# Kernel optimization log

Hardware: AMD Instinct MI355X
Metric: run time of the kernel (lower is better)

Reference implementation:

```python
import jax, jax.numpy as jnp
import numpy as np

D_MODEL = 1024
N_HEADS = 16
HEAD_DIM = D_MODEL // N_HEADS


def setup_inputs() -> dict:
    key = jax.random.key(0)
    k_x, k_qkv, k_proj = jax.random.split(key, 3)
    x = jax.random.normal(k_x, (2, 2048, D_MODEL), dtype=jnp.float32)
    # flax nnx.Linear kernels: shape (in_features, out_features), lecun_normal-ish scale
    w_qkv = jax.random.normal(k_qkv, (D_MODEL, 3 * D_MODEL), dtype=jnp.float32) / np.sqrt(D_MODEL)
    w_proj = jax.random.normal(k_proj, (D_MODEL, D_MODEL), dtype=jnp.float32) / np.sqrt(D_MODEL)
    return {"x": x, "w_qkv": w_qkv, "w_proj": w_proj}


def reference(x, w_qkv, w_proj):
    bsz, seq_len, d_model = x.shape
    qkv = x @ w_qkv  # (B, T, 3*D)
    q, k, v = jnp.split(qkv, 3, axis=-1)
    q = q.reshape(bsz, seq_len, N_HEADS, HEAD_DIM)
    k = k.reshape(bsz, seq_len, N_HEADS, HEAD_DIM)
    v = v.reshape(bsz, seq_len, N_HEADS, HEAD_DIM)
    scale = jnp.sqrt(jnp.asarray(HEAD_DIM, dtype=x.dtype))
    attn_logits = jnp.einsum('bthd,bshd->bhts', q / scale, k)  # (B, H, T, T)
    attn_weights = jax.nn.softmax(attn_logits, axis=-1)
    attn_out = jnp.einsum('bhts,bshd->bthd', attn_weights, v)
    attn_out = attn_out.reshape(bsz, seq_len, d_model)
    return attn_out @ w_proj
```

## Files before the change

kernel.cpp:

```cpp
#include <hip/hip_runtime.h>
#include <hip/hip_bf16.h>
#include <cmath>

#define D_MODEL 1024
#define NH 16
#define HD 64
#define BSZ 2
#define SEQ 2048
#define MTOT (BSZ * SEQ)

typedef _Float16 f16x8 __attribute__((ext_vector_type(8)));
typedef __fp16   fp16x2 __attribute__((ext_vector_type(2)));
typedef float    f32x4  __attribute__((ext_vector_type(4)));
typedef float    f32x16 __attribute__((ext_vector_type(16)));
typedef unsigned int uivec2 __attribute__((ext_vector_type(2)));

#define QSCALE 0.18033688011112042f

__device__ __forceinline__ ushort f2h(float x) {
    union { _Float16 h; ushort u; } cv;
    cv.h = (_Float16)x;
    return cv.u;
}
__device__ __forceinline__ uint pkh(float a, float b) {
    union { fp16x2 h; uint u; } cv;
    cv.h = __builtin_amdgcn_cvt_pkrtz(a, b);
    return cv.u;
}
__device__ __forceinline__ float fexp2(float x) {
    float r; asm("v_exp_f32 %0, %1" : "=v"(r) : "v"(x)); return r;
}
__device__ __forceinline__ float fmax3(float a, float b, float c) {
    return fmaxf(fmaxf(a, b), c);
}
__device__ __forceinline__ void gload_lds16(const ushort* g, ushort* l) {
    __builtin_amdgcn_global_load_lds(
        (const __attribute__((address_space(1))) void*)g,
        (__attribute__((address_space(3))) void*)l, 16, 0, 0);
}

__global__ __launch_bounds__(256)
void cast8(const float* __restrict__ in, ushort* __restrict__ out, int n)
{
    const int i = (blockIdx.x * 256 + threadIdx.x) * 8;
    if (i >= n) return;
    float4 a = *(const float4*)(in + i);
    float4 b = *(const float4*)(in + i + 4);
    alignas(16) ushort h8[8];
    h8[0] = f2h(a.x); h8[1] = f2h(a.y); h8[2] = f2h(a.z); h8[3] = f2h(a.w);
    h8[4] = f2h(b.x); h8[5] = f2h(b.y); h8[6] = f2h(b.z); h8[7] = f2h(b.w);
    *(uint4*)(out + i) = *(const uint4*)h8;
}

__global__ __launch_bounds__(256)
void transpose_cast2(const float* __restrict__ A, const float* __restrict__ B,
                     ushort* __restrict__ At, ushort* __restrict__ Bt)
{
    __shared__ float tile[32][33];
    const int z = blockIdx.z;
    const float* in = (z < 3) ? A : B;
    ushort* out     = (z < 3) ? At : Bt;
    const int C     = (z < 3) ? 3 * D_MODEL : D_MODEL;
    const int cb    = (z < 3) ? z * 32 + blockIdx.x : blockIdx.x;
    const int R = D_MODEL;
    const int t  = threadIdx.x;
    const int r0 = blockIdx.y * 32, c0 = cb * 32;
    const int tr = t >> 5, tc = t & 31;
#pragma unroll
    for (int s = 0; s < 4; ++s)
        tile[tr + 8 * s][tc] = in[(size_t)(r0 + tr + 8 * s) * C + c0 + tc];
    __syncthreads();
#pragma unroll
    for (int s = 0; s < 4; ++s)
        out[(size_t)(c0 + tr + 8 * s) * R + r0 + tc] = f2h(tile[tc][tr + 8 * s]);
}

template <int MODE>
__global__ __launch_bounds__(256)
void gemm_mfma(const ushort* __restrict__ A, const ushort* __restrict__ Bt,
               float* __restrict__ outp,
               ushort* __restrict__ Qw, ushort* __restrict__ Kw,
               ushort* __restrict__ Vw, int N)
{
    __shared__ ushort As[128 * 64];
    __shared__ ushort Bs[128 * 64];

    const int t  = threadIdx.x;
    const int w  = t >> 6;
    const int l  = t & 63;
    const int lr = l & 15;
    const int lg = l >> 4;
    const int wr = w >> 1, wc = w & 1;
    const int m0 = blockIdx.y * 128, n0 = blockIdx.x * 128;

    const int srow = l >> 3;
    const int scol = (l & 7) * 8;

    const ushort* Ab = A  + (size_t)m0 * 1024;
    const ushort* Bb = Bt + (size_t)n0 * 1024;

    f32x4 acc[4][4];
#pragma unroll
    for (int i = 0; i < 4; ++i)
#pragma unroll
        for (int j = 0; j < 4; ++j) acc[i][j] = (f32x4){0.f, 0.f, 0.f, 0.f};

    for (int k0 = 0; k0 < 1024; k0 += 64) {
#pragma unroll
        for (int i = 0; i < 4; ++i) {
            const int r8 = (w * 4 + i) * 8;
            gload_lds16(Ab + (size_t)(r8 + srow) * 1024 + k0 + scol, &As[r8 * 64]);
            gload_lds16(Bb + (size_t)(r8 + srow) * 1024 + k0 + scol, &Bs[r8 * 64]);
        }
        __syncthreads();

#pragma unroll
        for (int kk = 0; kk < 2; ++kk) {
            f16x8 af[4], bf[4];
#pragma unroll
            for (int m = 0; m < 4; ++m)
                af[m] = *(const f16x8*)&As[(wr * 64 + m * 16 + lr) * 64 + kk * 32 + lg * 8];
#pragma unroll
            for (int n = 0; n < 4; ++n)
                bf[n] = *(const f16x8*)&Bs[(wc * 64 + n * 16 + lr) * 64 + kk * 32 + lg * 8];
#pragma unroll
            for (int m = 0; m < 4; ++m)
#pragma unroll
                for (int n = 0; n < 4; ++n)
                    acc[m][n] = __builtin_amdgcn_mfma_f32_16x16x32_f16(
                        af[m], bf[n], acc[m][n], 0, 0, 0);
        }
        __syncthreads();
    }

    if (MODE == 1) {
#pragma unroll
        for (int mf = 0; mf < 4; ++mf) {
            const int row = m0 + wr * 64 + mf * 16 + lg * 4;
#pragma unroll
            for (int nf = 0; nf < 4; ++nf) {
                const int col = n0 + wc * 64 + nf * 16 + lr;
#pragma unroll
                for (int i = 0; i < 4; ++i)
                    outp[(size_t)(row + i) * N + col] = acc[mf][nf][i];
            }
        }
    } else {
#pragma unroll
        for (int mf = 0; mf < 4; ++mf) {
            const int row = m0 + wr * 64 + mf * 16 + lg * 4;
            const int b   = row >> 11;
            const int tt0 = row & (SEQ - 1);
#pragma unroll
            for (int nf = 0; nf < 4; ++nf) {
                const int col   = n0 + wc * 64 + nf * 16 + lr;
                const int which = col >> 10;
                const int h     = (col >> 6) & 15;
                const int d     = col & 63;
                if (which == 2) {
                    ushort* p = Vw + (((size_t)(b * NH + h) * HD + d) * SEQ) + tt0;
                    alignas(8) ushort e4[4];
#pragma unroll
                    for (int i = 0; i < 4; ++i) e4[i] = f2h(acc[mf][nf][i]);
                    *(uint2*)p = *(const uint2*)e4;
                } else {
                    ushort* dst = (which == 0) ? Qw : Kw;
                    const float sc = (which == 0) ? QSCALE : 1.0f;
#pragma unroll
                    for (int i = 0; i < 4; ++i)
                        dst[((size_t)(b * NH + h) * SEQ + tt0 + i) * HD + d] =
                            f2h(acc[mf][nf][i] * sc);
                }
            }
        }
    }
}

__global__ __launch_bounds__(512, 4)
void attn_mfma7(const ushort* __restrict__ Qw, const ushort* __restrict__ Kw,
                const ushort* __restrict__ Vtg, ushort* __restrict__ AO)
{
    __shared__ ushort KsAll[2][2][64 * 64];
    __shared__ ushort VtAll[2][2][64 * 64];

    const int t    = threadIdx.x;
    const int w    = t >> 6;
    const int l    = t & 63;
    const int q    = l & 31;
    const int hi   = l >> 5;
    const int half = w >> 2;
    const int ww   = w & 3;

    const int bh = blockIdx.y;
    const int q0 = blockIdx.x * 128 + ww * 32;
    const int kbase = half * (SEQ / 2);
    const int NT = (SEQ / 2) / 64;

    const ushort* Qp = Qw  + (size_t)bh * SEQ * HD;
    const ushort* Kp = Kw  + (size_t)bh * SEQ * HD;
    const ushort* Vp = Vtg + (size_t)bh * HD * SEQ;

    ushort (*Ks)[64 * 64] = KsAll[half];
    ushort (*Vt)[64 * 64] = VtAll[half];

    f16x8 qf[4];
#pragma unroll
    for (int kc = 0; kc < 4; ++kc)
        qf[kc] = *(const f16x8*)(Qp + (size_t)(q0 + q) * HD + kc * 16 + hi * 8);

    f32x16 oacc[2];
#pragma unroll
    for (int db = 0; db < 2; ++db)
#pragma unroll
        for (int r = 0; r < 16; ++r) oacc[db][r] = 0.f;
    float m_run = -3.0e38f, l_run = 0.f;

    auto stageK = [&](int buf, int k0) {
#pragma unroll
        for (int s = 0; s < 2; ++s) {
            const int c    = ww * 64 + l + 256 * s;
            const int row  = c >> 3;
            const int unit = (c & 7) ^ (row & 7);
            gload_lds16(Kp + (size_t)(k0 + row) * HD + unit * 8,
                        &Ks[buf][(ww * 64 + 256 * s) * 8]);
        }
    };
    auto stageV = [&](int buf, int k0) {
#pragma unroll
        for (int s = 0; s < 2; ++s) {
            const int c    = ww * 64 + l + 256 * s;
            const int row  = c >> 3;
            const int unit = (c & 7) ^ (row & 7);
            gload_lds16(Vp + (size_t)row * SEQ + k0 + unit * 8,
                        &Vt[buf][(ww * 64 + 256 * s) * 8]);
        }
    };

    stageK(0, kbase);
    stageV(0, kbase);
    __syncthreads();

    int cur = 0;
    for (int kt = 0; kt < NT; ++kt) {
        if (kt + 1 < NT) {
            stageK(cur ^ 1, kbase + (kt + 1) * 64);
            stageV(cur ^ 1, kbase + (kt + 1) * 64);
        }

        f32x16 sacc[2];
        __builtin_amdgcn_s_setprio(1);
#pragma unroll
        for (int kb = 0; kb < 2; ++kb) {
            f32x16 a;
#pragma unroll
            for (int r = 0; r < 16; ++r) a[r] = 0.f;
            const int row = kb * 32 + q;
            const int swz = (row & 7) << 4;
#pragma unroll
            for (int kc = 0; kc < 4; ++kc) {
                f16x8 kf = *(const f16x8*)(
                    (const char*)Ks[cur] + row * 128 + ((kc * 32 + hi * 16) ^ swz));
                a = __builtin_amdgcn_mfma_f32_32x32x16_f16(kf, qf[kc], a, 0, 0, 0);
            }
            sacc[kb] = a;
        }
        __builtin_amdgcn_s_setprio(0);

        float p0 = fmax3(fmaxf(sacc[0][0], sacc[1][0]),
                         fmaxf(sacc[0][1], sacc[1][1]),
                         fmaxf(sacc[0][2], sacc[1][2]));
        float p1 = fmax3(fmaxf(sacc[0][3], sacc[1][3]),
                         fmaxf(sacc[0][4], sacc[1][4]),
                         fmaxf(sacc[0][5], sacc[1][5]));
        float p2 = fmax3(fmaxf(sacc[0][6], sacc[1][6]),
                         fmaxf(sacc[0][7], sacc[1][7]),
                         fmaxf(sacc[0][8], sacc[1][8]));
        float p3 = fmax3(fmaxf(sacc[0][9], sacc[1][9]),
                         fmaxf(sacc[0][10], sacc[1][10]),
                         fmaxf(sacc[0][11], sacc[1][11]));
        float p4 = fmax3(fmaxf(sacc[0][12], sacc[1][12]),
                         fmaxf(sacc[0][13], sacc[1][13]),
                         fmaxf(sacc[0][14], sacc[1][14]));
        float p5 = fmaxf(sacc[0][15], sacc[1][15]);
        float mx = fmaxf(fmax3(p0, p1, p2), fmax3(p3, p4, p5));
        mx = fmaxf(mx, __shfl_xor(mx, 32));

        if (__any(mx > m_run + 8.0f)) {
            const float m_new = fmaxf(m_run, mx);
            const float scale = fexp2(m_run - m_new);
            m_run = m_new;
            l_run *= scale;
#pragma unroll
            for (int db = 0; db < 2; ++db)
#pragma unroll
                for (int r = 0; r < 16; ++r) oacc[db][r] *= scale;
        }

#pragma unroll
        for (int kb = 0; kb < 2; ++kb)
#pragma unroll
            for (int r = 0; r < 16; ++r)
                sacc[kb][r] = fexp2(sacc[kb][r] - m_run);

        float ts[16];
#pragma unroll
        for (int r = 0; r < 16; ++r) ts[r] = sacc[0][r] + sacc[1][r];
#pragma unroll
        for (int s = 8; s > 0; s >>= 1)
#pragma unroll
            for (int r = 0; r < 8; ++r)
                if (r < s) ts[r] += ts[r + s];
        l_run += ts[0] + __shfl_xor(ts[0], 32);

        f16x8 pfrag[4];
#pragma unroll
        for (int kb = 0; kb < 2; ++kb)
#pragma unroll
            for (int lc = 0; lc < 2; ++lc) {
                const int rb = lc * 8;
                uint a = pkh(sacc[kb][rb + 0], sacc[kb][rb + 1]);
                uint b = pkh(sacc[kb][rb + 2], sacc[kb][rb + 3]);
                uint c = pkh(sacc[kb][rb + 4], sacc[kb][rb + 5]);
                uint d = pkh(sacc[kb][rb + 6], sacc[kb][rb + 7]);
                uivec2 r0 = __builtin_amdgcn_permlane32_swap(a, c, false, false);
                uivec2 r1 = __builtin_amdgcn_permlane32_swap(b, d, false, false);
                union { uint u[4]; f16x8 v; } f;
                f.u[0] = r0.x;
                f.u[1] = r1.x;
                f.u[2] = r0.y;
                f.u[3] = r1.y;
                pfrag[kb * 2 + lc] = f.v;
            }

        __builtin_amdgcn_s_setprio(1);
#pragma unroll
        for (int db = 0; db < 2; ++db) {
            const int row = db * 32 + q;
            const int swz = (row & 7) << 4;
#pragma unroll
            for (int kc = 0; kc < 4; ++kc) {
                f16x8 vf = *(const f16x8*)(
                    (const char*)Vt[cur] + row * 128 + ((kc * 32 + hi * 16) ^ swz));
                oacc[db] = __builtin_amdgcn_mfma_f32_32x32x16_f16(
                    vf, pfrag[kc], oacc[db], 0, 0, 0);
            }
        }
        __builtin_amdgcn_s_setprio(0);

        __syncthreads();
        cur ^= 1;
    }

    float* oex = (float*)KsAll;
    float* mex = (float*)VtAll;
    float* lex = mex + 256;

    if (half == 1) {
        mex[ww * 64 + l] = m_run;
        lex[ww * 64 + l] = l_run;
#pragma unroll
        for (int db = 0; db < 2; ++db)
#pragma unroll
            for (int r = 0; r < 16; ++r)
                oex[(((ww * 2 + db) * 16) + r) * 64 + l] = oacc[db][r];
    }
    __syncthreads();
    if (half == 0) {
        const float m2 = mex[ww * 64 + l];
        const float l2 = lex[ww * 64 + l];
        const float mf = fmaxf(m_run, m2);
        float w1 = fexp2(m_run - mf), w2 = fexp2(m2 - mf);
        const float inv = 1.f / (l_run * w1 + l2 * w2);
        w1 *= inv; w2 *= inv;

        const int b = bh >> 4, h = bh & 15;
        ushort* orow = AO + ((size_t)(b * SEQ) + q0 + q) * D_MODEL + h * HD;
#pragma unroll
        for (int db = 0; db < 2; ++db)
#pragma unroll
            for (int g = 0; g < 4; ++g) {
                const int d = db * 32 + g * 8 + hi * 4;
                alignas(8) ushort e4[4];
#pragma unroll
                for (int i = 0; i < 4; ++i) {
                    const float o2 = oex[(((ww * 2 + db) * 16) + g * 4 + i) * 64 + l];
                    e4[i] = f2h(oacc[db][g * 4 + i] * w1 + o2 * w2);
                }
                *(uint2*)(orow + d) = *(const uint2*)e4;
            }
    }
}

extern "C" void kernel_launch(void* const* d_in, const int* in_sizes, int n_in,
                              void* d_out, int out_size, void* d_ws, size_t ws_size,
                              hipStream_t stream)
{
    const float* x      = (const float*)d_in[0];
    const float* w_qkv  = (const float*)d_in[1];
    const float* w_proj = (const float*)d_in[2];
    float* out = (float*)d_out;

    ushort* Xh  = (ushort*)d_ws;
    ushort* WqT = Xh  + (size_t)MTOT * D_MODEL;
    ushort* WpT = WqT + (size_t)3 * D_MODEL * D_MODEL;
    ushort* Qw  = WpT + (size_t)D_MODEL * D_MODEL;
    ushort* Kw  = Qw  + (size_t)MTOT * D_MODEL;
    ushort* Vt  = Kw  + (size_t)MTOT * D_MODEL;
    ushort* AOh = Vt  + (size_t)MTOT * D_MODEL;

    dim3 blk(256);

    cast8<<<dim3(MTOT * D_MODEL / (8 * 256)), blk, 0, stream>>>(x, Xh, MTOT * D_MODEL);
    transpose_cast2<<<dim3(32, 32, 4), blk, 0, stream>>>(w_qkv, w_proj, WqT, WpT);

    gemm_mfma<0><<<dim3(3 * D_MODEL / 128, MTOT / 128), blk, 0, stream>>>(
        Xh, WqT, nullptr, Qw, Kw, Vt, 3 * D_MODEL);

    attn_mfma7<<<dim3(SEQ / 128, BSZ * NH), dim3(512), 0, stream>>>(Qw, Kw, Vt, AOh);

    gemm_mfma<1><<<dim3(D_MODEL / 128, MTOT / 128), blk, 0, stream>>>(
        AOh, WpT, out, nullptr, nullptr, nullptr, D_MODEL);
}
```

Measured before the change: 142.5 us.

## Double-buffer GEMM LDS tiles with K=32 stages to overlap loads and MFMA

```diff
diff --git a/kernel.cpp b/kernel.cpp
--- a/kernel.cpp
+++ b/kernel.cpp
@@ -82,8 +82,8 @@
                ushort* __restrict__ Qw, ushort* __restrict__ Kw,
                ushort* __restrict__ Vw, int N)
 {
-    __shared__ ushort As[128 * 64];
-    __shared__ ushort Bs[128 * 64];
+    __shared__ ushort As[2][128 * 32];
+    __shared__ ushort Bs[2][128 * 32];
 
     const int t  = threadIdx.x;
     const int w  = t >> 6;
@@ -93,9 +93,6 @@
     const int wr = w >> 1, wc = w & 1;
     const int m0 = blockIdx.y * 128, n0 = blockIdx.x * 128;
 
-    const int srow = l >> 3;
-    const int scol = (l & 7) * 8;
-
     const ushort* Ab = A  + (size_t)m0 * 1024;
     const ushort* Bb = Bt + (size_t)n0 * 1024;
 
@@ -105,32 +102,43 @@
 #pragma unroll
         for (int j = 0; j < 4; ++j) acc[i][j] = (f32x4){0.f, 0.f, 0.f, 0.f};
 
-    for (int k0 = 0; k0 < 1024; k0 += 64) {
-#pragma unroll
-        for (int i = 0; i < 4; ++i) {
-            const int r8 = (w * 4 + i) * 8;
-            gload_lds16(Ab + (size_t)(r8 + srow) * 1024 + k0 + scol, &As[r8 * 64]);
-            gload_lds16(Bb + (size_t)(r8 + srow) * 1024 + k0 + scol, &Bs[r8 * 64]);
-        }
+    auto stage = [&](int buf, int k0) {
+#pragma unroll
+        for (int s = 0; s < 2; ++s) {
+            const int c    = s * 64 + l;
+            const int row  = w * 32 + (c >> 2);
+            const int unit = c & 3;
+            gload_lds16(Ab + (size_t)row * 1024 + k0 + unit * 8,
+                        &As[buf][(w * 128 + s * 64) * 8]);
+            gload_lds16(Bb + (size_t)row * 1024 + k0 + unit * 8,
+                        &Bs[buf][(w * 128 + s * 64) * 8]);
+        }
+    };
+
+    stage(0, 0);
+    __syncthreads();
+
+    int cur = 0;
+#pragma unroll 4
+    for (int kt = 0; kt < 32; ++kt) {
+        if (kt + 1 < 32) stage(cur ^ 1, (kt + 1) * 32);
+
+        f16x8 af[4], bf[4];
+#pragma unroll
+        for (int m = 0; m < 4; ++m)
+            af[m] = *(const f16x8*)&As[cur][(wr * 64 + m * 16 + lr) * 32 + lg * 8];
+#pragma unroll
+        for (int n = 0; n < 4; ++n)
+            bf[n] = *(const f16x8*)&Bs[cur][(wc * 64 + n * 16 + lr) * 32 + lg * 8];
+#pragma unroll
+        for (int m = 0; m < 4; ++m)
+#pragma unroll
+            for (int n = 0; n < 4; ++n)
+                acc[m][n] = __builtin_amdgcn_mfma_f32_16x16x32_f16(
+                    af[m], bf[n], acc[m][n], 0, 0, 0);
+
         __syncthreads();
-
-#pragma unroll
-        for (int kk = 0; kk < 2; ++kk) {
-            f16x8 af[4], bf[4];
-#pragma unroll
-            for (int m = 0; m < 4; ++m)
-                af[m] = *(const f16x8*)&As[(wr * 64 + m * 16 + lr) * 64 + kk * 32 + lg * 8];
-#pragma unroll
-            for (int n = 0; n < 4; ++n)
-                bf[n] = *(const f16x8*)&Bs[(wc * 64 + n * 16 + lr) * 64 + kk * 32 + lg * 8];
-#pragma unroll
-            for (int m = 0; m < 4; ++m)
-#pragma unroll
-                for (int n = 0; n < 4; ++n)
-                    acc[m][n] = __builtin_amdgcn_mfma_f32_16x16x32_f16(
-                        af[m], bf[n], acc[m][n], 0, 0, 0);
-        }
-        __syncthreads();
+        cur ^= 1;
     }
 
     if (MODE == 1) {
```

Result: no change. 143.8 us (+0.9%).
